# Kernel optimization log

Hardware: AMD Instinct MI355X
Metric: run time of the kernel (lower is better)

## Reference

```python
import jax, jax.numpy as jnp
import numpy as np

N, P, S = 512, 2048, 128  # diagrams, max points per diagram, phi samples


def setup_inputs() -> dict:
    key = jax.random.key(0)
    k1, k2, k3 = jax.random.split(key, 3)
    births = jax.random.uniform(k1, (N, P), dtype=jnp.float32)
    pers = jax.random.uniform(k2, (N, P), dtype=jnp.float32)
    diagrams = jnp.stack([births, births + pers], axis=-1)  # (N, P, 2) with death >= birth
    # ragged structure: each diagram has a variable number of valid points
    lens = jax.random.randint(k3, (N,), P // 4, P + 1)
    mask = jnp.arange(P)[None, :] < lens[:, None]  # bool (N, P)
    samples = jnp.linspace(0.0, 2.0, S, dtype=jnp.float32)
    theta = jnp.array([20.0], dtype=jnp.float32)
    constant = jnp.array([1.0], dtype=jnp.float32)
    power = jnp.array([1.0], dtype=jnp.float32)
    return {"diagrams": diagrams, "mask": mask, "samples": samples,
            "theta": theta, "constant": constant, "power": power}


def reference(diagrams, mask, samples, theta, constant, power):
    # phi = FlatPerslayPhi: sigmoid of a tent function evaluated at S sample points
    xs = diagrams[..., 0:1]  # (N, P, 1) births
    ys = diagrams[..., 1:2]  # (N, P, 1) deaths
    th = theta[0]
    # vector: (N, P, S)
    vector = jax.nn.sigmoid(th * (0.5 * (ys - xs)
                                  - jnp.abs(samples[None, None, :] - 0.5 * (ys + xs))))
    # weight = PowerPerslayWeight: constant * |death - birth| ** power, (N, P)
    w = constant[0] * jnp.power(jnp.abs(diagrams[..., 1] - diagrams[..., 0]), power[0])
    # ragged padding contributes 0 to the sum reduction
    w = jnp.where(mask, w, jnp.zeros_like(w))
    vector = vector * w[..., None]  # weight broadcast over phi output dims
    out = jnp.sum(vector, axis=1)   # perm_op = reduce_sum over points -> (N, S)
    return out                       # rho = identity
```

## Files before the change

kernel.cpp:

```cpp
#include <hip/hip_runtime.h>

#ifndef __has_builtin
#define __has_builtin(x) 0
#endif

#if __has_builtin(__builtin_amdgcn_exp2f)
#define FAST_EXP2(x) __builtin_amdgcn_exp2f(x)
#else
#define FAST_EXP2(x) exp2f(x)
#endif
#if __has_builtin(__builtin_amdgcn_rcpf)
#define FAST_RCP(x) __builtin_amdgcn_rcpf(x)
#else
#define FAST_RCP(x) (1.0f / (x))
#endif

#define P_PTS 2048
#define S_SAMP 128
#define NTH 512
#define NG 32
#define KS 8

__global__ __launch_bounds__(NTH, 4) void perslay_kernel(
    const float* __restrict__ diagrams,
    const void*  __restrict__ maskp,
    const float* __restrict__ samples,
    const float* __restrict__ theta,
    const float* __restrict__ constant,
    const float* __restrict__ power,
    float* __restrict__ out)
{
    __shared__ float4 pts[P_PTS];
    __shared__ int    woff[33];

    const int n    = blockIdx.x;
    const int tid  = threadIdx.x;
    const int lane = tid & 63;
    const int wid  = tid >> 6;

    const float th  = theta[0];
    const float cst = constant[0];
    const float pw  = power[0];
    const float c   = th * 1.4426950408889634f;

    const unsigned int* mw = (const unsigned int*)maskp;
    const bool isByte = (mw[0] > 1u) | (mw[1] > 1u) | (mw[2] > 1u) | (mw[3] > 1u);

    const float2* __restrict__ dg = ((const float2*)diagrams) + (size_t)n * P_PTS;

    float4 val[4];
    int    rank[4];
    bool   valid[4];

    #pragma unroll
    for (int r = 0; r < 4; ++r) {
        const int p = r * NTH + tid;
        const float2 xy = dg[p];
        bool m;
        if (isByte) m = ((const unsigned char*)maskp)[(size_t)n * P_PTS + p] != 0;
        else        m = ((const int*)maskp)[(size_t)n * P_PTS + p] != 0;
        const float pers = xy.y - xy.x;
        const float ap   = fabsf(pers);
        float w;
        if (pw == 1.0f)      w = cst * ap;
        else if (pw == 2.0f) w = cst * ap * ap;
        else                 w = cst * powf(ap, pw);
        valid[r] = m && (w != 0.0f);
        const float A = FAST_EXP2(-c * xy.y);
        const float B = FAST_EXP2( c * xy.x);
        val[r] = make_float4(A, B, w, 0.0f);
        const unsigned long long b = __ballot(valid[r] ? 1 : 0);
        if (lane == 0) woff[r * 8 + wid] = (int)__popcll(b);
        rank[r] = (int)__popcll(b & ((1ull << lane) - 1ull));
    }
    __syncthreads();

    if (tid == 0) {
        int run = 0;
        #pragma unroll
        for (int j = 0; j < 32; ++j) { const int t = woff[j]; woff[j] = run; run += t; }
        woff[32] = run;
    }
    __syncthreads();

    #pragma unroll
    for (int r = 0; r < 4; ++r)
        if (valid[r]) pts[woff[r * 8 + wid] + rank[r]] = val[r];
    const int cnt    = woff[32];
    const int padded = (cnt + NG - 1) & ~(NG - 1);
    if (tid < padded - cnt) pts[cnt + tid] = make_float4(0.0f, 0.0f, 0.0f, 0.0f);
    __syncthreads();

    const int   g     = tid >> 4;
    const int   sbase = tid & 15;

    float E[KS], rE[KS], acc[KS];
    #pragma unroll
    for (int k = 0; k < KS; ++k) {
        const float sv = samples[sbase + 16 * k];
        E[k]  = FAST_EXP2( c * sv);
        rE[k] = FAST_EXP2(-c * sv);
        acc[k] = 0.0f;
    }

    const int jmax = padded >> 5;
    const float4* __restrict__ pbase = pts + g;

#define INNER_LOOP(SELFN)                                          \
    _Pragma("unroll 2")                                            \
    for (int j = 0; j < jmax; ++j) {                               \
        const float4 v = pbase[j * NG];                            \
        _Pragma("unroll")                                          \
        for (int k = 0; k < KS; ++k) {                             \
            const float t1 = E[k]  * v.x;                          \
            const float t2 = rE[k] * v.y;                          \
            const float u  = 1.0f + SELFN(t1, t2);                 \
            acc[k] = fmaf(v.z, FAST_RCP(u), acc[k]);               \
        }                                                          \
    }

    if (c >= 0.0f) { INNER_LOOP(fmaxf) } else { INNER_LOOP(fminf) }
#undef INNER_LOOP

    __syncthreads();
    float* part = (float*)pts;
    #pragma unroll
    for (int k = 0; k < KS; ++k)
        part[g * S_SAMP + sbase + 16 * k] = acc[k];
    __syncthreads();

    float* part2 = part + NG * S_SAMP;
    {
        const int s  = tid & (S_SAMP - 1);
        const int cq = tid >> 7;
        float t = 0.0f;
        #pragma unroll
        for (int gg = 0; gg < 8; ++gg)
            t += part[(cq * 8 + gg) * S_SAMP + s];
        part2[cq * S_SAMP + s] = t;
    }
    __syncthreads();

    if (tid < S_SAMP) {
        out[(size_t)n * S_SAMP + tid] =
            (part2[tid] + part2[S_SAMP + tid]) +
            (part2[2 * S_SAMP + tid] + part2[3 * S_SAMP + tid]);
    }
}

extern "C" void kernel_launch(void* const* d_in, const int* in_sizes, int n_in,
                              void* d_out, int out_size, void* d_ws, size_t ws_size,
                              hipStream_t stream) {
    const float* diagrams = (const float*)d_in[0];
    const void*  mask     = d_in[1];
    const float* samples  = (const float*)d_in[2];
    const float* theta    = (const float*)d_in[3];
    const float* constant = (const float*)d_in[4];
    const float* power    = (const float*)d_in[5];
    float* out = (float*)d_out;

    const int N = in_sizes[0] / (2 * P_PTS);
    perslay_kernel<<<N, NTH, 0, stream>>>(diagrams, mask, samples, theta,
                                          constant, power, out);
}
```

Before: 92.07 us.

## Split each diagram into four point chunks with a separate reduction kernel

Each diagram's points are now split into four chunks of 512, each handled by a 256-thread block, so the grid grows from N to 4N blocks. Partial sums go to workspace, and a second small kernel adds the four partials per output. The aim is better load balance across CUs, since ragged diagrams leave some large blocks idle, and more blocks to fill the machine. The cost is an extra kernel launch, a workspace round trip, and more per-point padding overhead across chunks.

```diff
diff --git a/kernel.cpp b/kernel.cpp
--- a/kernel.cpp
+++ b/kernel.cpp
@@ -17,23 +17,26 @@
 
 #define P_PTS 2048
 #define S_SAMP 128
-#define NTH 512
-#define NG 32
+#define CHUNK 512
+#define CH 4
+#define NTH 256
+#define NG 16
 #define KS 8
 
-__global__ __launch_bounds__(NTH, 4) void perslay_kernel(
+__global__ __launch_bounds__(NTH, 8) void perslay_part_kernel(
     const float* __restrict__ diagrams,
     const void*  __restrict__ maskp,
     const float* __restrict__ samples,
     const float* __restrict__ theta,
     const float* __restrict__ constant,
     const float* __restrict__ power,
-    float* __restrict__ out)
+    float* __restrict__ ws)
 {
-    __shared__ float4 pts[P_PTS];
-    __shared__ int    woff[33];
+    __shared__ float4 pts[CHUNK];
+    __shared__ int    woff[9];
 
-    const int n    = blockIdx.x;
+    const int n    = blockIdx.x >> 2;
+    const int ch   = blockIdx.x & 3;
     const int tid  = threadIdx.x;
     const int lane = tid & 63;
     const int wid  = tid >> 6;
@@ -46,19 +49,20 @@
     const unsigned int* mw = (const unsigned int*)maskp;
     const bool isByte = (mw[0] > 1u) | (mw[1] > 1u) | (mw[2] > 1u) | (mw[3] > 1u);
 
-    const float2* __restrict__ dg = ((const float2*)diagrams) + (size_t)n * P_PTS;
+    const size_t pbase_g = (size_t)n * P_PTS + (size_t)ch * CHUNK;
+    const float2* __restrict__ dg = ((const float2*)diagrams) + pbase_g;
 
-    float4 val[4];
-    int    rank[4];
-    bool   valid[4];
+    float4 val[2];
+    int    rank[2];
+    bool   valid[2];
 
     #pragma unroll
-    for (int r = 0; r < 4; ++r) {
+    for (int r = 0; r < 2; ++r) {
         const int p = r * NTH + tid;
         const float2 xy = dg[p];
         bool m;
-        if (isByte) m = ((const unsigned char*)maskp)[(size_t)n * P_PTS + p] != 0;
-        else        m = ((const int*)maskp)[(size_t)n * P_PTS + p] != 0;
+        if (isByte) m = ((const unsigned char*)maskp)[pbase_g + p] != 0;
+        else        m = ((const int*)maskp)[pbase_g + p] != 0;
         const float pers = xy.y - xy.x;
         const float ap   = fabsf(pers);
         float w;
@@ -70,7 +74,7 @@
         const float B = FAST_EXP2( c * xy.x);
         val[r] = make_float4(A, B, w, 0.0f);
         const unsigned long long b = __ballot(valid[r] ? 1 : 0);
-        if (lane == 0) woff[r * 8 + wid] = (int)__popcll(b);
+        if (lane == 0) woff[r * 4 + wid] = (int)__popcll(b);
         rank[r] = (int)__popcll(b & ((1ull << lane) - 1ull));
     }
     __syncthreads();
@@ -78,15 +82,15 @@
     if (tid == 0) {
         int run = 0;
         #pragma unroll
-        for (int j = 0; j < 32; ++j) { const int t = woff[j]; woff[j] = run; run += t; }
-        woff[32] = run;
+        for (int j = 0; j < 8; ++j) { const int t = woff[j]; woff[j] = run; run += t; }
+        woff[8] = run;
     }
     __syncthreads();
 
     #pragma unroll
-    for (int r = 0; r < 4; ++r)
-        if (valid[r]) pts[woff[r * 8 + wid] + rank[r]] = val[r];
-    const int cnt    = woff[32];
+    for (int r = 0; r < 2; ++r)
+        if (valid[r]) pts[woff[r * 4 + wid] + rank[r]] = val[r];
+    const int cnt    = woff[8];
     const int padded = (cnt + NG - 1) & ~(NG - 1);
     if (tid < padded - cnt) pts[cnt + tid] = make_float4(0.0f, 0.0f, 0.0f, 0.0f);
     __syncthreads();
@@ -103,13 +107,13 @@
         acc[k] = 0.0f;
     }
 
-    const int jmax = padded >> 5;
-    const float4* __restrict__ pbase = pts + g;
+    const int jmax = padded >> 4;
+    const float4* __restrict__ pb = pts + g;
 
 #define INNER_LOOP(SELFN)                                          \
     _Pragma("unroll 2")                                            \
     for (int j = 0; j < jmax; ++j) {                               \
-        const float4 v = pbase[j * NG];                            \
+        const float4 v = pb[j * NG];                               \
         _Pragma("unroll")                                          \
         for (int k = 0; k < KS; ++k) {                             \
             const float t1 = E[k]  * v.x;                          \
@@ -129,22 +133,25 @@
         part[g * S_SAMP + sbase + 16 * k] = acc[k];
     __syncthreads();
 
-    float* part2 = part + NG * S_SAMP;
-    {
-        const int s  = tid & (S_SAMP - 1);
-        const int cq = tid >> 7;
+    if (tid < S_SAMP) {
         float t = 0.0f;
         #pragma unroll
-        for (int gg = 0; gg < 8; ++gg)
-            t += part[(cq * 8 + gg) * S_SAMP + s];
-        part2[cq * S_SAMP + s] = t;
+        for (int gg = 0; gg < NG; ++gg) t += part[gg * S_SAMP + tid];
+        ws[(size_t)blockIdx.x * S_SAMP + tid] = t;
     }
-    __syncthreads();
+}
 
-    if (tid < S_SAMP) {
-        out[(size_t)n * S_SAMP + tid] =
-            (part2[tid] + part2[S_SAMP + tid]) +
-            (part2[2 * S_SAMP + tid] + part2[3 * S_SAMP + tid]);
+__global__ __launch_bounds__(256) void perslay_reduce_kernel(
+    const float* __restrict__ part,
+    float* __restrict__ out,
+    int total)
+{
+    const int idx = blockIdx.x * 256 + threadIdx.x;
+    if (idx < total) {
+        const int n = idx >> 7;
+        const int s = idx & (S_SAMP - 1);
+        const float* p = part + (size_t)n * CH * S_SAMP + s;
+        out[idx] = (p[0] + p[S_SAMP]) + (p[2 * S_SAMP] + p[3 * S_SAMP]);
     }
 }
 
@@ -158,8 +165,11 @@
     const float* constant = (const float*)d_in[4];
     const float* power    = (const float*)d_in[5];
     float* out = (float*)d_out;
+    float* ws  = (float*)d_ws;
 
     const int N = in_sizes[0] / (2 * P_PTS);
-    perslay_kernel<<<N, NTH, 0, stream>>>(diagrams, mask, samples, theta,
-                                          constant, power, out);
+    perslay_part_kernel<<<N * CH, NTH, 0, stream>>>(diagrams, mask, samples,
+                                                    theta, constant, power, ws);
+    const int total = N * S_SAMP;
+    perslay_reduce_kernel<<<(total + 255) / 256, 256, 0, stream>>>(ws, out, total);
 }
```

Result: slower. 93.94 us (+2.0%).
